# Performance work log

Hardware: AMD Instinct MI355X
Metric: run time of the kernel (lower is better)

Reference implementation:

```python
import jax, jax.numpy as jnp
import numpy as np

L1 = 1e-3  # init kwarg l1
EPS_NORM = 1e-12  # torch F.normalize eps


def _l2_normalize(x):
    # F.normalize(x, p=2, dim=1)
    n = jnp.linalg.norm(x, axis=1, keepdims=True)
    return x / jnp.maximum(n, EPS_NORM)


def _rbf_kernel(x):
    # x: [n, d]
    x2 = jnp.sum(x * x, axis=1, keepdims=True)          # [n,1]
    dist = x2 + x2.T - 2.0 * (x @ x.T)                   # [n,n]
    dist = jnp.maximum(dist, 0.0)
    # torch.median on even-size input returns the LOWER middle element
    flat = jnp.sort(jax.lax.stop_gradient(dist).ravel())
    median_dist = flat[(flat.shape[0] - 1) // 2]
    sigma2 = median_dist + 1e-5
    return jnp.exp(-dist / (2.0 * sigma2))


def _hsic(x, y):
    # x, y: [n, d]. Note: original normalizes in forward AND in hsic; L2
    # normalization is idempotent, so one normalize here is exact.
    x = _l2_normalize(x)
    y = _l2_normalize(y)
    K = _rbf_kernel(x)
    L = _rbf_kernel(y)
    n = K.shape[0]
    # K @ H with H = I - 1/n  ==  K - row_mean(K)
    KH = K - jnp.mean(K, axis=1, keepdims=True)
    LH = L - jnp.mean(L, axis=1, keepdims=True)
    return jnp.sum(KH * LH.T) / float((n - 1) ** 2)


def setup_inputs() -> dict:
    key = jax.random.key(0)
    k1, k2, k3, k4 = jax.random.split(key, 4)
    N, D = 65536, 512     # patches, feature dim
    K_INST, NS = 256, 32  # instances, samples per instance (== max_bg_samples)
    dp = jax.random.normal(k1, (N, D), dtype=jnp.float32)
    gate = jax.random.normal(k2, (N, D), dtype=jnp.float32)
    inst_idx = jax.random.randint(k3, (K_INST, NS), 0, N, dtype=jnp.int64)
    bg_idx = jax.random.randint(k4, (K_INST, NS), 0, N, dtype=jnp.int64)
    return {"dp": dp, "gate": gate, "inst_idx": inst_idx, "bg_idx": bg_idx}


def reference(dp, gate, inst_idx, bg_idx):
    x = dp[inst_idx]   # [K, n, d] per-instance foreground samples
    bg = dp[bg_idx]    # [K, n, d] per-instance background samples
    hs = jax.vmap(_hsic)(x, bg)  # [K]
    return jnp.mean(hs) + L1 * jnp.mean(jnp.abs(gate))
```

## Files before the change

### kernel.cpp

```cpp
#include <hip/hip_runtime.h>
#include <hip/hip_bf16.h>

#define NS 32
#define FD 512
#define K_INST 256
#define CHUNK 256
#define C4 (CHUNK/4)
#define PADF 260
#define PAD4 (PADF/4)
#define MPAD 33
#define GATE_BLOCKS 1024
#define GATE_N4 (65536*512/4)

__device__ __forceinline__ float wave_reduce_add(float v) {
  for (int off = 32; off; off >>= 1) v += __shfl_down(v, off, 64);
  return v;
}

__global__ __launch_bounds__(256) void fused_kernel(
    const float* __restrict__ dp, const float* __restrict__ gate,
    const int* __restrict__ inst_idx, const int* __restrict__ bg_idx,
    float* __restrict__ ws_gate, float* __restrict__ ws_hs) {

  __shared__ float sX[NS * PADF];
  __shared__ float sDist[NS * MPAD];
  __shared__ float sMat[2][NS * MPAD];
  __shared__ float sRowM[2][NS];
  __shared__ float sInv[NS];
  __shared__ float sN2[NS];
  __shared__ int   sIdx[NS];
  __shared__ int   sHist[256];
  __shared__ int   sWaveSum[4];
  __shared__ float sWaveRed[4];
  __shared__ unsigned sPrefix;
  __shared__ int   sWant;

  const int tid  = threadIdx.x;
  const int bid  = blockIdx.x;
  const int lane = tid & 63;
  const int wave = tid >> 6;

  if (bid >= K_INST) {
    const int gb = bid - K_INST;
    const float4* g4 = reinterpret_cast<const float4*>(gate);
    float s = 0.f;
    for (size_t i = (size_t)gb * 256 + tid; i < (size_t)GATE_N4; i += (size_t)GATE_BLOCKS * 256) {
      float4 v = g4[i];
      s += fabsf(v.x) + fabsf(v.y) + fabsf(v.z) + fabsf(v.w);
    }
    s = wave_reduce_add(s);
    if (lane == 0) sWaveRed[wave] = s;
    __syncthreads();
    if (tid == 0) ws_gate[gb] = sWaveRed[0] + sWaveRed[1] + sWaveRed[2] + sWaveRed[3];
    return;
  }

  const int k  = bid;
  const int ti = tid >> 4;
  const int tj = tid & 15;
  const float4* sX4 = reinterpret_cast<const float4*>(sX);

  for (int m = 0; m < 2; ++m) {
    const int* idx = (m == 0 ? inst_idx : bg_idx) + k * NS;
    if (tid < NS) sIdx[tid] = idx[tid];
    __syncthreads();

    float a00 = 0.f, a01 = 0.f, a10 = 0.f, a11 = 0.f;
    for (int ch = 0; ch < 2; ++ch) {
      for (int q = tid; q < NS * C4; q += 256) {
        int r = q >> 6, c = q & 63;
        float4 v = *(reinterpret_cast<const float4*>(dp + (size_t)sIdx[r] * FD + ch * CHUNK) + c);
        *(reinterpret_cast<float4*>(&sX[r * PADF]) + c) = v;
      }
      __syncthreads();
      #pragma unroll 4
      for (int c = 0; c < C4; ++c) {
        float4 x0 = sX4[ti * PAD4 + c];
        float4 x1 = sX4[(ti + 16) * PAD4 + c];
        float4 y0 = sX4[tj * PAD4 + c];
        float4 y1 = sX4[(tj + 16) * PAD4 + c];
        a00 += x0.x*y0.x + x0.y*y0.y + x0.z*y0.z + x0.w*y0.w;
        a01 += x0.x*y1.x + x0.y*y1.y + x0.z*y1.z + x0.w*y1.w;
        a10 += x1.x*y0.x + x1.y*y0.y + x1.z*y0.z + x1.w*y0.w;
        a11 += x1.x*y1.x + x1.y*y1.y + x1.z*y1.z + x1.w*y1.w;
      }
      __syncthreads();
    }

    if (ti == tj) { sN2[ti] = a00; sN2[ti + 16] = a11; }
    __syncthreads();
    if (tid < NS) sInv[tid] = 1.f / fmaxf(sqrtf(sN2[tid]), 1e-12f);
    __syncthreads();

    {
      float i0 = sInv[ti], i1 = sInv[ti + 16], j0 = sInv[tj], j1 = sInv[tj + 16];
      sDist[ti * MPAD + tj]             = (ti == tj) ? 0.f : fmaxf(2.f - 2.f * a00 * i0 * j0, 0.f);
      sDist[ti * MPAD + (tj + 16)]      = fmaxf(2.f - 2.f * a01 * i0 * j1, 0.f);
      sDist[(ti + 16) * MPAD + tj]      = fmaxf(2.f - 2.f * a10 * i1 * j0, 0.f);
      sDist[(ti + 16) * MPAD + (tj + 16)] = (ti == tj) ? 0.f : fmaxf(2.f - 2.f * a11 * i1 * j1, 0.f);
    }
    if (tid == 0) { sPrefix = 0u; sWant = (NS * NS - 1) / 2; }
    __syncthreads();

    for (int shift = 24; shift >= 0; shift -= 8) {
      sHist[tid] = 0;
      __syncthreads();
      unsigned pref = sPrefix;
      int want = sWant;
      unsigned hi_mask = (shift == 24) ? 0u : (0xFFFFFFFFu << (shift + 8));
      for (int q = tid; q < NS * NS; q += 256) {
        unsigned u = __float_as_uint(sDist[(q >> 5) * MPAD + (q & 31)]);
        if ((u & hi_mask) == pref) atomicAdd(&sHist[(u >> shift) & 255], 1);
      }
      __syncthreads();
      int v = sHist[tid];
      int x = v;
      for (int off = 1; off < 64; off <<= 1) {
        int y = __shfl_up(x, off, 64);
        if (lane >= off) x += y;
      }
      if (lane == 63) sWaveSum[wave] = x;
      __syncthreads();
      int add = 0;
      for (int w = 0; w < wave; ++w) add += sWaveSum[w];
      x += add;
      int ex = x - v;
      if (ex <= want && want < ex + v) {
        sPrefix = pref | ((unsigned)tid << shift);
        sWant   = want - ex;
      }
      __syncthreads();
    }
    float sigma2 = __uint_as_float(sPrefix) + 1e-5f;

    for (int q = tid; q < NS * NS; q += 256) {
      int i = q >> 5, j = q & 31;
      sMat[m][i * MPAD + j] = expf(-sDist[i * MPAD + j] / (2.f * sigma2));
    }
    __syncthreads();

    {
      int r = tid >> 3, g = tid & 7;
      float p = 0.f;
      for (int s = 0; s < 4; ++s) p += sMat[m][r * MPAD + g + 8 * s];
      for (int off = 4; off; off >>= 1) p += __shfl_down(p, off, 8);
      if (g == 0) sRowM[m][r] = p * (1.f / 32.f);
    }
    __syncthreads();
  }

  float part = 0.f;
  for (int q = tid; q < NS * NS; q += 256) {
    int i = q >> 5, j = q & 31;
    part += (sMat[0][i * MPAD + j] - sRowM[0][i]) * (sMat[1][i * MPAD + j] - sRowM[1][j]);
  }
  part = wave_reduce_add(part);
  if (lane == 0) sWaveRed[wave] = part;
  __syncthreads();
  if (tid == 0)
    ws_hs[k] = (sWaveRed[0] + sWaveRed[1] + sWaveRed[2] + sWaveRed[3]) * (1.f / 961.f);
}

__global__ __launch_bounds__(256) void final_kernel(
    const float* __restrict__ ws_gate, const float* __restrict__ ws_hs,
    float* __restrict__ out) {
  __shared__ float sW[8];
  const int tid = threadIdx.x, lane = tid & 63, wave = tid >> 6;
  float g = 0.f;
  for (int i = tid; i < GATE_BLOCKS; i += 256) g += ws_gate[i];
  g = wave_reduce_add(g);
  if (lane == 0) sW[wave] = g;
  float h = (tid < K_INST) ? ws_hs[tid] : 0.f;
  h = wave_reduce_add(h);
  if (lane == 0) sW[4 + wave] = h;
  __syncthreads();
  if (tid == 0) {
    float gsum = sW[0] + sW[1] + sW[2] + sW[3];
    float hsum = sW[4] + sW[5] + sW[6] + sW[7];
    out[0] = hsum * (1.f / 256.f) + 1e-3f * (gsum / (65536.f * 512.f));
  }
}

extern "C" void kernel_launch(void* const* d_in, const int* in_sizes, int n_in,
                              void* d_out, int out_size, void* d_ws, size_t ws_size,
                              hipStream_t stream) {
  const float* dp   = (const float*)d_in[0];
  const float* gate = (const float*)d_in[1];
  const int*   inst = (const int*)d_in[2];
  const int*   bg   = (const int*)d_in[3];
  float* out = (float*)d_out;
  float* ws  = (float*)d_ws;
  float* ws_gate = ws;
  float* ws_hs   = ws + GATE_BLOCKS;

  fused_kernel<<<K_INST + GATE_BLOCKS, 256, 0, stream>>>(dp, gate, inst, bg, ws_gate, ws_hs);
  final_kernel<<<1, 256, 0, stream>>>(ws_gate, ws_hs, out);
}
```

Before: 43.43 us.

## Fuse final reduction via last-block counter and restructure Gram tile computation

Replaces the separate final reduction kernel with a last-block-done atomic counter inside the fused kernel; a memset of the counter is added instead. The Gram matrix computation is restructured: each wave handles a quarter of the feature columns with a 4x4 register tile per lane, using an XOR-swizzled unpadded shared layout, register prefetch of the second feature chunk during the first chunk's compute, and a cross-wave partial-sum reduction. The gate loop gets a fixed trip count with unrolling. This trades an extra memset launch and more registers for one fewer kernel launch and better load/compute overlap.

```diff
diff --git a/kernel.cpp b/kernel.cpp
--- a/kernel.cpp
+++ b/kernel.cpp
@@ -5,11 +5,8 @@
 #define FD 512
 #define K_INST 256
 #define CHUNK 256
-#define C4 (CHUNK/4)
-#define PADF 260
-#define PAD4 (PADF/4)
-#define MPAD 33
 #define GATE_BLOCKS 1024
+#define TOTAL_BLOCKS (K_INST + GATE_BLOCKS)
 #define GATE_N4 (65536*512/4)
 
 __device__ __forceinline__ float wave_reduce_add(float v) {
@@ -20,164 +17,215 @@
 __global__ __launch_bounds__(256) void fused_kernel(
     const float* __restrict__ dp, const float* __restrict__ gate,
     const int* __restrict__ inst_idx, const int* __restrict__ bg_idx,
-    float* __restrict__ ws_gate, float* __restrict__ ws_hs) {
-
-  __shared__ float sX[NS * PADF];
-  __shared__ float sDist[NS * MPAD];
-  __shared__ float sMat[2][NS * MPAD];
-  __shared__ float sRowM[2][NS];
-  __shared__ float sInv[NS];
-  __shared__ float sN2[NS];
-  __shared__ int   sIdx[NS];
-  __shared__ int   sHist[256];
-  __shared__ int   sWaveSum[4];
-  __shared__ float sWaveRed[4];
+    int* __restrict__ ctr,
+    float* __restrict__ ws_gate, float* __restrict__ ws_hs,
+    float* __restrict__ out) {
+
+  __shared__ float4 sX4[NS * 64];
+  __shared__ float  sGD[NS * NS];
+  __shared__ float  sMat[2][NS * NS];
+  __shared__ float  sRowM[2][NS];
+  __shared__ float  sInv[NS];
+  __shared__ int    sIdx[NS];
+  __shared__ int    sHist[256];
+  __shared__ int    sWaveSum[4];
+  __shared__ float  sWaveRed[8];
   __shared__ unsigned sPrefix;
-  __shared__ int   sWant;
+  __shared__ int    sWant;
+  __shared__ int    sLast;
+
+  float* sPartF = reinterpret_cast<float*>(sX4);
 
   const int tid  = threadIdx.x;
   const int bid  = blockIdx.x;
   const int lane = tid & 63;
-  const int wave = tid >> 6;
+  const int w    = tid >> 6;
 
   if (bid >= K_INST) {
     const int gb = bid - K_INST;
     const float4* g4 = reinterpret_cast<const float4*>(gate);
     float s = 0.f;
-    for (size_t i = (size_t)gb * 256 + tid; i < (size_t)GATE_N4; i += (size_t)GATE_BLOCKS * 256) {
-      float4 v = g4[i];
+    size_t base = (size_t)gb * 256 + tid;
+    #pragma unroll 4
+    for (int it = 0; it < 32; ++it) {
+      float4 v = g4[base + (size_t)it * (GATE_BLOCKS * 256)];
       s += fabsf(v.x) + fabsf(v.y) + fabsf(v.z) + fabsf(v.w);
     }
     s = wave_reduce_add(s);
-    if (lane == 0) sWaveRed[wave] = s;
+    if (lane == 0) sWaveRed[w] = s;
     __syncthreads();
     if (tid == 0) ws_gate[gb] = sWaveRed[0] + sWaveRed[1] + sWaveRed[2] + sWaveRed[3];
-    return;
-  }
-
-  const int k  = bid;
-  const int ti = tid >> 4;
-  const int tj = tid & 15;
-  const float4* sX4 = reinterpret_cast<const float4*>(sX);
-
-  for (int m = 0; m < 2; ++m) {
-    const int* idx = (m == 0 ? inst_idx : bg_idx) + k * NS;
-    if (tid < NS) sIdx[tid] = idx[tid];
-    __syncthreads();
-
-    float a00 = 0.f, a01 = 0.f, a10 = 0.f, a11 = 0.f;
-    for (int ch = 0; ch < 2; ++ch) {
-      for (int q = tid; q < NS * C4; q += 256) {
-        int r = q >> 6, c = q & 63;
-        float4 v = *(reinterpret_cast<const float4*>(dp + (size_t)sIdx[r] * FD + ch * CHUNK) + c);
-        *(reinterpret_cast<float4*>(&sX[r * PADF]) + c) = v;
-      }
-      __syncthreads();
+  } else {
+    const int k  = bid;
+    const int li = lane >> 3;
+    const int lj = lane & 7;
+
+    for (int m = 0; m < 2; ++m) {
+      const int* idx = (m == 0 ? inst_idx : bg_idx) + k * NS;
+      if (tid < NS) sIdx[tid] = idx[tid];
+      __syncthreads();
+
+      float acc[4][4];
+      #pragma unroll
+      for (int a = 0; a < 4; ++a)
+        #pragma unroll
+        for (int b = 0; b < 4; ++b) acc[a][b] = 0.f;
+
+      float4 pre[8];
+      #pragma unroll
+      for (int kk = 0; kk < 8; ++kk) {
+        int r = w + 4 * kk;
+        pre[kk] = *(reinterpret_cast<const float4*>(dp + (size_t)sIdx[r] * FD) + lane);
+      }
+      #pragma unroll
+      for (int kk = 0; kk < 8; ++kk) {
+        int r = w + 4 * kk;
+        sX4[r * 64 + (lane ^ (r & 7))] = pre[kk];
+      }
+      __syncthreads();
+      #pragma unroll
+      for (int kk = 0; kk < 8; ++kk) {
+        int r = w + 4 * kk;
+        pre[kk] = *(reinterpret_cast<const float4*>(dp + (size_t)sIdx[r] * FD + CHUNK) + lane);
+      }
       #pragma unroll 4
-      for (int c = 0; c < C4; ++c) {
-        float4 x0 = sX4[ti * PAD4 + c];
-        float4 x1 = sX4[(ti + 16) * PAD4 + c];
-        float4 y0 = sX4[tj * PAD4 + c];
-        float4 y1 = sX4[(tj + 16) * PAD4 + c];
-        a00 += x0.x*y0.x + x0.y*y0.y + x0.z*y0.z + x0.w*y0.w;
-        a01 += x0.x*y1.x + x0.y*y1.y + x0.z*y1.z + x0.w*y1.w;
-        a10 += x1.x*y0.x + x1.y*y0.y + x1.z*y0.z + x1.w*y0.w;
-        a11 += x1.x*y1.x + x1.y*y1.y + x1.z*y1.z + x1.w*y1.w;
-      }
-      __syncthreads();
-    }
-
-    if (ti == tj) { sN2[ti] = a00; sN2[ti + 16] = a11; }
-    __syncthreads();
-    if (tid < NS) sInv[tid] = 1.f / fmaxf(sqrtf(sN2[tid]), 1e-12f);
-    __syncthreads();
-
-    {
-      float i0 = sInv[ti], i1 = sInv[ti + 16], j0 = sInv[tj], j1 = sInv[tj + 16];
-      sDist[ti * MPAD + tj]             = (ti == tj) ? 0.f : fmaxf(2.f - 2.f * a00 * i0 * j0, 0.f);
-      sDist[ti * MPAD + (tj + 16)]      = fmaxf(2.f - 2.f * a01 * i0 * j1, 0.f);
-      sDist[(ti + 16) * MPAD + tj]      = fmaxf(2.f - 2.f * a10 * i1 * j0, 0.f);
-      sDist[(ti + 16) * MPAD + (tj + 16)] = (ti == tj) ? 0.f : fmaxf(2.f - 2.f * a11 * i1 * j1, 0.f);
-    }
-    if (tid == 0) { sPrefix = 0u; sWant = (NS * NS - 1) / 2; }
-    __syncthreads();
-
-    for (int shift = 24; shift >= 0; shift -= 8) {
-      sHist[tid] = 0;
-      __syncthreads();
-      unsigned pref = sPrefix;
-      int want = sWant;
-      unsigned hi_mask = (shift == 24) ? 0u : (0xFFFFFFFFu << (shift + 8));
-      for (int q = tid; q < NS * NS; q += 256) {
-        unsigned u = __float_as_uint(sDist[(q >> 5) * MPAD + (q & 31)]);
-        if ((u & hi_mask) == pref) atomicAdd(&sHist[(u >> shift) & 255], 1);
-      }
-      __syncthreads();
-      int v = sHist[tid];
-      int x = v;
-      for (int off = 1; off < 64; off <<= 1) {
-        int y = __shfl_up(x, off, 64);
-        if (lane >= off) x += y;
-      }
-      if (lane == 63) sWaveSum[wave] = x;
-      __syncthreads();
-      int add = 0;
-      for (int w = 0; w < wave; ++w) add += sWaveSum[w];
-      x += add;
-      int ex = x - v;
-      if (ex <= want && want < ex + v) {
-        sPrefix = pref | ((unsigned)tid << shift);
-        sWant   = want - ex;
-      }
-      __syncthreads();
-    }
-    float sigma2 = __uint_as_float(sPrefix) + 1e-5f;
-
+      for (int c = 16 * w; c < 16 * w + 16; ++c) {
+        float4 xs[4], ys[4];
+        #pragma unroll
+        for (int s = 0; s < 4; ++s) {
+          xs[s] = sX4[(li + 8 * s) * 64 + (c ^ li)];
+          ys[s] = sX4[(lj + 8 * s) * 64 + (c ^ lj)];
+        }
+        #pragma unroll
+        for (int a = 0; a < 4; ++a)
+          #pragma unroll
+          for (int b = 0; b < 4; ++b)
+            acc[a][b] += xs[a].x * ys[b].x + xs[a].y * ys[b].y
+                       + xs[a].z * ys[b].z + xs[a].w * ys[b].w;
+      }
+      __syncthreads();
+      #pragma unroll
+      for (int kk = 0; kk < 8; ++kk) {
+        int r = w + 4 * kk;
+        sX4[r * 64 + (lane ^ (r & 7))] = pre[kk];
+      }
+      __syncthreads();
+      #pragma unroll 4
+      for (int c = 16 * w; c < 16 * w + 16; ++c) {
+        float4 xs[4], ys[4];
+        #pragma unroll
+        for (int s = 0; s < 4; ++s) {
+          xs[s] = sX4[(li + 8 * s) * 64 + (c ^ li)];
+          ys[s] = sX4[(lj + 8 * s) * 64 + (c ^ lj)];
+        }
+        #pragma unroll
+        for (int a = 0; a < 4; ++a)
+          #pragma unroll
+          for (int b = 0; b < 4; ++b)
+            acc[a][b] += xs[a].x * ys[b].x + xs[a].y * ys[b].y
+                       + xs[a].z * ys[b].z + xs[a].w * ys[b].w;
+      }
+      __syncthreads();
+      #pragma unroll
+      for (int a = 0; a < 4; ++a)
+        #pragma unroll
+        for (int b = 0; b < 4; ++b) {
+          int A = li + 8 * a, B = lj + 8 * b;
+          sPartF[w * 1024 + A * 32 + (B ^ ((A & 3) << 3))] = acc[a][b];
+        }
+      __syncthreads();
+      for (int p = tid; p < 1024; p += 256) {
+        float s = sPartF[p] + sPartF[1024 + p] + sPartF[2048 + p] + sPartF[3072 + p];
+        int A = p >> 5, Bx = p & 31;
+        sGD[A * 32 + (Bx ^ ((A & 3) << 3))] = s;
+      }
+      __syncthreads();
+      if (tid < NS) sInv[tid] = 1.f / fmaxf(sqrtf(sGD[tid * 33]), 1e-12f);
+      __syncthreads();
+      for (int p = tid; p < 1024; p += 256) {
+        int i = p >> 5, j = p & 31;
+        sGD[p] = (i == j) ? 0.f
+                          : fmaxf(2.f - 2.f * sGD[p] * sInv[i] * sInv[j], 0.f);
+      }
+      if (tid == 0) { sPrefix = 0u; sWant = (NS * NS - 1) / 2; }
+      __syncthreads();
+
+      for (int shift = 24; shift >= 0; shift -= 8) {
+        sHist[tid] = 0;
+        __syncthreads();
+        unsigned pref = sPrefix;
+        int want = sWant;
+        unsigned hi_mask = (shift == 24) ? 0u : (0xFFFFFFFFu << (shift + 8));
+        for (int q = tid; q < NS * NS; q += 256) {
+          unsigned u = __float_as_uint(sGD[q]);
+          if ((u & hi_mask) == pref) atomicAdd(&sHist[(u >> shift) & 255], 1);
+        }
+        __syncthreads();
+        int v = sHist[tid];
+        int x = v;
+        for (int off = 1; off < 64; off <<= 1) {
+          int y = __shfl_up(x, off, 64);
+          if (lane >= off) x += y;
+        }
+        if (lane == 63) sWaveSum[w] = x;
+        __syncthreads();
+        int add = 0;
+        for (int ww = 0; ww < w; ++ww) add += sWaveSum[ww];
+        x += add;
+        int ex = x - v;
+        if (ex <= want && want < ex + v) {
+          sPrefix = pref | ((unsigned)tid << shift);
+          sWant   = want - ex;
+        }
+        __syncthreads();
+      }
+      float sigma2 = __uint_as_float(sPrefix) + 1e-5f;
+
+      for (int q = tid; q < NS * NS; q += 256)
+        sMat[m][q] = expf(-sGD[q] / (2.f * sigma2));
+      __syncthreads();
+      {
+        int r = tid >> 3, g = tid & 7;
+        float p = 0.f;
+        for (int s = 0; s < 4; ++s) p += sMat[m][r * 32 + g + 8 * s];
+        for (int off = 4; off; off >>= 1) p += __shfl_down(p, off, 8);
+        if (g == 0) sRowM[m][r] = p * (1.f / 32.f);
+      }
+      __syncthreads();
+    }
+
+    float part = 0.f;
     for (int q = tid; q < NS * NS; q += 256) {
       int i = q >> 5, j = q & 31;
-      sMat[m][i * MPAD + j] = expf(-sDist[i * MPAD + j] / (2.f * sigma2));
-    }
+      part += (sMat[0][q] - sRowM[0][i]) * (sMat[1][q] - sRowM[1][j]);
+    }
+    part = wave_reduce_add(part);
+    if (lane == 0) sWaveRed[w] = part;
     __syncthreads();
-
-    {
-      int r = tid >> 3, g = tid & 7;
-      float p = 0.f;
-      for (int s = 0; s < 4; ++s) p += sMat[m][r * MPAD + g + 8 * s];
-      for (int off = 4; off; off >>= 1) p += __shfl_down(p, off, 8);
-      if (g == 0) sRowM[m][r] = p * (1.f / 32.f);
-    }
+    if (tid == 0)
+      ws_hs[k] = (sWaveRed[0] + sWaveRed[1] + sWaveRed[2] + sWaveRed[3]) * (1.f / 961.f);
+  }
+
+  if (tid == 0) {
+    __threadfence();
+    sLast = (atomicAdd(ctr, 1) == TOTAL_BLOCKS - 1) ? 1 : 0;
+  }
+  __syncthreads();
+  if (sLast) {
+    __threadfence();
+    float g = 0.f;
+    for (int i = tid; i < GATE_BLOCKS; i += 256) g += ws_gate[i];
+    g = wave_reduce_add(g);
+    if (lane == 0) sWaveRed[w] = g;
+    float h = (tid < K_INST) ? ws_hs[tid] : 0.f;
+    h = wave_reduce_add(h);
+    if (lane == 0) sWaveRed[4 + w] = h;
     __syncthreads();
-  }
-
-  float part = 0.f;
-  for (int q = tid; q < NS * NS; q += 256) {
-    int i = q >> 5, j = q & 31;
-    part += (sMat[0][i * MPAD + j] - sRowM[0][i]) * (sMat[1][i * MPAD + j] - sRowM[1][j]);
-  }
-  part = wave_reduce_add(part);
-  if (lane == 0) sWaveRed[wave] = part;
-  __syncthreads();
-  if (tid == 0)
-    ws_hs[k] = (sWaveRed[0] + sWaveRed[1] + sWaveRed[2] + sWaveRed[3]) * (1.f / 961.f);
-}
-
-__global__ __launch_bounds__(256) void final_kernel(
-    const float* __restrict__ ws_gate, const float* __restrict__ ws_hs,
-    float* __restrict__ out) {
-  __shared__ float sW[8];
-  const int tid = threadIdx.x, lane = tid & 63, wave = tid >> 6;
-  float g = 0.f;
-  for (int i = tid; i < GATE_BLOCKS; i += 256) g += ws_gate[i];
-  g = wave_reduce_add(g);
-  if (lane == 0) sW[wave] = g;
-  float h = (tid < K_INST) ? ws_hs[tid] : 0.f;
-  h = wave_reduce_add(h);
-  if (lane == 0) sW[4 + wave] = h;
-  __syncthreads();
-  if (tid == 0) {
-    float gsum = sW[0] + sW[1] + sW[2] + sW[3];
-    float hsum = sW[4] + sW[5] + sW[6] + sW[7];
-    out[0] = hsum * (1.f / 256.f) + 1e-3f * (gsum / (65536.f * 512.f));
+    if (tid == 0) {
+      float gsum = sWaveRed[0] + sWaveRed[1] + sWaveRed[2] + sWaveRed[3];
+      float hsum = sWaveRed[4] + sWaveRed[5] + sWaveRed[6] + sWaveRed[7];
+      out[0] = hsum * (1.f / 256.f) + 1e-3f * (gsum / (65536.f * 512.f));
+    }
   }
 }
 
@@ -190,9 +238,10 @@
   const int*   bg   = (const int*)d_in[3];
   float* out = (float*)d_out;
   float* ws  = (float*)d_ws;
-  float* ws_gate = ws;
-  float* ws_hs   = ws + GATE_BLOCKS;
-
-  fused_kernel<<<K_INST + GATE_BLOCKS, 256, 0, stream>>>(dp, gate, inst, bg, ws_gate, ws_hs);
-  final_kernel<<<1, 256, 0, stream>>>(ws_gate, ws_hs, out);
+  int*   ctr = (int*)d_ws;
+  float* ws_gate = ws + 16;
+  float* ws_hs   = ws + 16 + GATE_BLOCKS;
+
+  hipMemsetAsync(d_ws, 0, 4, stream);
+  fused_kernel<<<TOTAL_BLOCKS, 256, 0, stream>>>(dp, gate, inst, bg, ctr, ws_gate, ws_hs, out);
 }
```

Result: slower. 84.12 us (+93.7%).

## Split HSIC per-matrix work across two blocks and add contraction kernel

Applied to the files above, without the earlier changes.

Each instance's K and L kernel-matrix computations now run in separate blocks (512 HSIC blocks instead of 256), which halves the serial per-block chain of gather, Gram, radix median select and exp. The resulting 32x32 matrices and row means are written to workspace, and a new contract_kernel computes the centered HSIC sum per instance. This exposes more parallelism on the long-latency HSIC path. The cost is an extra kernel launch plus a round trip of about 2 MB through global memory.

```diff
diff --git a/kernel.cpp b/kernel.cpp
--- a/kernel.cpp
+++ b/kernel.cpp
@@ -9,6 +9,7 @@
 #define PADF 260
 #define PAD4 (PADF/4)
 #define MPAD 33
+#define HSIC_BLOCKS 512
 #define GATE_BLOCKS 1024
 #define GATE_N4 (65536*512/4)
 
@@ -20,12 +21,12 @@
 __global__ __launch_bounds__(256) void fused_kernel(
     const float* __restrict__ dp, const float* __restrict__ gate,
     const int* __restrict__ inst_idx, const int* __restrict__ bg_idx,
-    float* __restrict__ ws_gate, float* __restrict__ ws_hs) {
+    float* __restrict__ ws_gate, float* __restrict__ ws_mats,
+    float* __restrict__ ws_means) {
 
   __shared__ float sX[NS * PADF];
-  __shared__ float sDist[NS * MPAD];
-  __shared__ float sMat[2][NS * MPAD];
-  __shared__ float sRowM[2][NS];
+  __shared__ float sD[NS * MPAD];
+  __shared__ float sRowM[NS];
   __shared__ float sInv[NS];
   __shared__ float sN2[NS];
   __shared__ int   sIdx[NS];
@@ -38,10 +39,10 @@
   const int tid  = threadIdx.x;
   const int bid  = blockIdx.x;
   const int lane = tid & 63;
-  const int wave = tid >> 6;
-
-  if (bid >= K_INST) {
-    const int gb = bid - K_INST;
+  const int w    = tid >> 6;
+
+  if (bid >= HSIC_BLOCKS) {
+    const int gb = bid - HSIC_BLOCKS;
     const float4* g4 = reinterpret_cast<const float4*>(gate);
     float s = 0.f;
     for (size_t i = (size_t)gb * 256 + tid; i < (size_t)GATE_N4; i += (size_t)GATE_BLOCKS * 256) {
@@ -49,113 +50,129 @@
       s += fabsf(v.x) + fabsf(v.y) + fabsf(v.z) + fabsf(v.w);
     }
     s = wave_reduce_add(s);
-    if (lane == 0) sWaveRed[wave] = s;
+    if (lane == 0) sWaveRed[w] = s;
     __syncthreads();
     if (tid == 0) ws_gate[gb] = sWaveRed[0] + sWaveRed[1] + sWaveRed[2] + sWaveRed[3];
     return;
   }
 
-  const int k  = bid;
+  const int k = bid >> 1;
+  const int m = bid & 1;
   const int ti = tid >> 4;
   const int tj = tid & 15;
   const float4* sX4 = reinterpret_cast<const float4*>(sX);
 
-  for (int m = 0; m < 2; ++m) {
-    const int* idx = (m == 0 ? inst_idx : bg_idx) + k * NS;
-    if (tid < NS) sIdx[tid] = idx[tid];
-    __syncthreads();
-
-    float a00 = 0.f, a01 = 0.f, a10 = 0.f, a11 = 0.f;
-    for (int ch = 0; ch < 2; ++ch) {
-      for (int q = tid; q < NS * C4; q += 256) {
-        int r = q >> 6, c = q & 63;
-        float4 v = *(reinterpret_cast<const float4*>(dp + (size_t)sIdx[r] * FD + ch * CHUNK) + c);
-        *(reinterpret_cast<float4*>(&sX[r * PADF]) + c) = v;
-      }
-      __syncthreads();
-      #pragma unroll 4
-      for (int c = 0; c < C4; ++c) {
-        float4 x0 = sX4[ti * PAD4 + c];
-        float4 x1 = sX4[(ti + 16) * PAD4 + c];
-        float4 y0 = sX4[tj * PAD4 + c];
-        float4 y1 = sX4[(tj + 16) * PAD4 + c];
-        a00 += x0.x*y0.x + x0.y*y0.y + x0.z*y0.z + x0.w*y0.w;
-        a01 += x0.x*y1.x + x0.y*y1.y + x0.z*y1.z + x0.w*y1.w;
-        a10 += x1.x*y0.x + x1.y*y0.y + x1.z*y0.z + x1.w*y0.w;
-        a11 += x1.x*y1.x + x1.y*y1.y + x1.z*y1.z + x1.w*y1.w;
-      }
-      __syncthreads();
-    }
-
-    if (ti == tj) { sN2[ti] = a00; sN2[ti + 16] = a11; }
-    __syncthreads();
-    if (tid < NS) sInv[tid] = 1.f / fmaxf(sqrtf(sN2[tid]), 1e-12f);
-    __syncthreads();
-
-    {
-      float i0 = sInv[ti], i1 = sInv[ti + 16], j0 = sInv[tj], j1 = sInv[tj + 16];
-      sDist[ti * MPAD + tj]             = (ti == tj) ? 0.f : fmaxf(2.f - 2.f * a00 * i0 * j0, 0.f);
-      sDist[ti * MPAD + (tj + 16)]      = fmaxf(2.f - 2.f * a01 * i0 * j1, 0.f);
-      sDist[(ti + 16) * MPAD + tj]      = fmaxf(2.f - 2.f * a10 * i1 * j0, 0.f);
-      sDist[(ti + 16) * MPAD + (tj + 16)] = (ti == tj) ? 0.f : fmaxf(2.f - 2.f * a11 * i1 * j1, 0.f);
-    }
-    if (tid == 0) { sPrefix = 0u; sWant = (NS * NS - 1) / 2; }
-    __syncthreads();
-
-    for (int shift = 24; shift >= 0; shift -= 8) {
-      sHist[tid] = 0;
-      __syncthreads();
-      unsigned pref = sPrefix;
-      int want = sWant;
-      unsigned hi_mask = (shift == 24) ? 0u : (0xFFFFFFFFu << (shift + 8));
-      for (int q = tid; q < NS * NS; q += 256) {
-        unsigned u = __float_as_uint(sDist[(q >> 5) * MPAD + (q & 31)]);
-        if ((u & hi_mask) == pref) atomicAdd(&sHist[(u >> shift) & 255], 1);
-      }
-      __syncthreads();
-      int v = sHist[tid];
-      int x = v;
-      for (int off = 1; off < 64; off <<= 1) {
-        int y = __shfl_up(x, off, 64);
-        if (lane >= off) x += y;
-      }
-      if (lane == 63) sWaveSum[wave] = x;
-      __syncthreads();
-      int add = 0;
-      for (int w = 0; w < wave; ++w) add += sWaveSum[w];
-      x += add;
-      int ex = x - v;
-      if (ex <= want && want < ex + v) {
-        sPrefix = pref | ((unsigned)tid << shift);
-        sWant   = want - ex;
-      }
-      __syncthreads();
-    }
-    float sigma2 = __uint_as_float(sPrefix) + 1e-5f;
-
+  const int* idx = (m == 0 ? inst_idx : bg_idx) + k * NS;
+  if (tid < NS) sIdx[tid] = idx[tid];
+  __syncthreads();
+
+  float a00 = 0.f, a01 = 0.f, a10 = 0.f, a11 = 0.f;
+  for (int ch = 0; ch < 2; ++ch) {
+    for (int q = tid; q < NS * C4; q += 256) {
+      int r = q >> 6, c = q & 63;
+      float4 v = *(reinterpret_cast<const float4*>(dp + (size_t)sIdx[r] * FD + ch * CHUNK) + c);
+      *(reinterpret_cast<float4*>(&sX[r * PADF]) + c) = v;
+    }
+    __syncthreads();
+    #pragma unroll 4
+    for (int c = 0; c < C4; ++c) {
+      float4 x0 = sX4[ti * PAD4 + c];
+      float4 x1 = sX4[(ti + 16) * PAD4 + c];
+      float4 y0 = sX4[tj * PAD4 + c];
+      float4 y1 = sX4[(tj + 16) * PAD4 + c];
+      a00 += x0.x*y0.x + x0.y*y0.y + x0.z*y0.z + x0.w*y0.w;
+      a01 += x0.x*y1.x + x0.y*y1.y + x0.z*y1.z + x0.w*y1.w;
+      a10 += x1.x*y0.x + x1.y*y0.y + x1.z*y0.z + x1.w*y0.w;
+      a11 += x1.x*y1.x + x1.y*y1.y + x1.z*y1.z + x1.w*y1.w;
+    }
+    __syncthreads();
+  }
+
+  if (ti == tj) { sN2[ti] = a00; sN2[ti + 16] = a11; }
+  __syncthreads();
+  if (tid < NS) sInv[tid] = 1.f / fmaxf(sqrtf(sN2[tid]), 1e-12f);
+  __syncthreads();
+
+  {
+    float i0 = sInv[ti], i1 = sInv[ti + 16], j0 = sInv[tj], j1 = sInv[tj + 16];
+    sD[ti * MPAD + tj]               = (ti == tj) ? 0.f : fmaxf(2.f - 2.f * a00 * i0 * j0, 0.f);
+    sD[ti * MPAD + (tj + 16)]        = fmaxf(2.f - 2.f * a01 * i0 * j1, 0.f);
+    sD[(ti + 16) * MPAD + tj]        = fmaxf(2.f - 2.f * a10 * i1 * j0, 0.f);
+    sD[(ti + 16) * MPAD + (tj + 16)] = (ti == tj) ? 0.f : fmaxf(2.f - 2.f * a11 * i1 * j1, 0.f);
+  }
+  if (tid == 0) { sPrefix = 0u; sWant = (NS * NS - 1) / 2; }
+  __syncthreads();
+
+  for (int shift = 24; shift >= 0; shift -= 8) {
+    sHist[tid] = 0;
+    __syncthreads();
+    unsigned pref = sPrefix;
+    int want = sWant;
+    unsigned hi_mask = (shift == 24) ? 0u : (0xFFFFFFFFu << (shift + 8));
     for (int q = tid; q < NS * NS; q += 256) {
-      int i = q >> 5, j = q & 31;
-      sMat[m][i * MPAD + j] = expf(-sDist[i * MPAD + j] / (2.f * sigma2));
-    }
-    __syncthreads();
-
-    {
-      int r = tid >> 3, g = tid & 7;
-      float p = 0.f;
-      for (int s = 0; s < 4; ++s) p += sMat[m][r * MPAD + g + 8 * s];
-      for (int off = 4; off; off >>= 1) p += __shfl_down(p, off, 8);
-      if (g == 0) sRowM[m][r] = p * (1.f / 32.f);
-    }
-    __syncthreads();
-  }
-
+      unsigned u = __float_as_uint(sD[(q >> 5) * MPAD + (q & 31)]);
+      if ((u & hi_mask) == pref) atomicAdd(&sHist[(u >> shift) & 255], 1);
+    }
+    __syncthreads();
+    int v = sHist[tid];
+    int x = v;
+    for (int off = 1; off < 64; off <<= 1) {
+      int y = __shfl_up(x, off, 64);
+      if (lane >= off) x += y;
+    }
+    if (lane == 63) sWaveSum[w] = x;
+    __syncthreads();
+    int add = 0;
+    for (int ww = 0; ww < w; ++ww) add += sWaveSum[ww];
+    x += add;
+    int ex = x - v;
+    if (ex <= want && want < ex + v) {
+      sPrefix = pref | ((unsigned)tid << shift);
+      sWant   = want - ex;
+    }
+    __syncthreads();
+  }
+  float sigma2 = __uint_as_float(sPrefix) + 1e-5f;
+
+  for (int q = tid; q < NS * NS; q += 256) {
+    int i = q >> 5, j = q & 31;
+    sD[i * MPAD + j] = expf(-sD[i * MPAD + j] / (2.f * sigma2));
+  }
+  __syncthreads();
+
+  {
+    int r = tid >> 3, g = tid & 7;
+    float p = 0.f;
+    for (int s = 0; s < 4; ++s) p += sD[r * MPAD + g + 8 * s];
+    for (int off = 4; off; off >>= 1) p += __shfl_down(p, off, 8);
+    if (g == 0) sRowM[r] = p * (1.f / 32.f);
+  }
+  __syncthreads();
+
+  float* mat = ws_mats + (size_t)bid * 1024;
+  for (int q = tid; q < NS * NS; q += 256)
+    mat[q] = sD[(q >> 5) * MPAD + (q & 31)];
+  if (tid < NS) ws_means[bid * NS + tid] = sRowM[tid];
+}
+
+__global__ __launch_bounds__(256) void contract_kernel(
+    const float* __restrict__ ws_mats, const float* __restrict__ ws_means,
+    float* __restrict__ ws_hs) {
+  __shared__ float sRM[2][NS];
+  __shared__ float sWaveRed[4];
+  const int k = blockIdx.x;
+  const int tid = threadIdx.x, lane = tid & 63, w = tid >> 6;
+  const float* Km = ws_mats + (size_t)(k * 2 + 0) * 1024;
+  const float* Lm = ws_mats + (size_t)(k * 2 + 1) * 1024;
+  if (tid < 64) sRM[tid >> 5][tid & 31] = ws_means[(k * 2 + (tid >> 5)) * NS + (tid & 31)];
+  __syncthreads();
   float part = 0.f;
   for (int q = tid; q < NS * NS; q += 256) {
     int i = q >> 5, j = q & 31;
-    part += (sMat[0][i * MPAD + j] - sRowM[0][i]) * (sMat[1][i * MPAD + j] - sRowM[1][j]);
+    part += (Km[q] - sRM[0][i]) * (Lm[q] - sRM[1][j]);
   }
   part = wave_reduce_add(part);
-  if (lane == 0) sWaveRed[wave] = part;
+  if (lane == 0) sWaveRed[w] = part;
   __syncthreads();
   if (tid == 0)
     ws_hs[k] = (sWaveRed[0] + sWaveRed[1] + sWaveRed[2] + sWaveRed[3]) * (1.f / 961.f);
@@ -190,9 +207,13 @@
   const int*   bg   = (const int*)d_in[3];
   float* out = (float*)d_out;
   float* ws  = (float*)d_ws;
-  float* ws_gate = ws;
-  float* ws_hs   = ws + GATE_BLOCKS;
-
-  fused_kernel<<<K_INST + GATE_BLOCKS, 256, 0, stream>>>(dp, gate, inst, bg, ws_gate, ws_hs);
+  float* ws_gate  = ws;
+  float* ws_hs    = ws + 1024;
+  float* ws_means = ws + 1024 + 256;
+  float* ws_mats  = ws + 1024 + 256 + 512 * 32;
+
+  fused_kernel<<<HSIC_BLOCKS + GATE_BLOCKS, 256, 0, stream>>>(
+      dp, gate, inst, bg, ws_gate, ws_mats, ws_means);
+  contract_kernel<<<K_INST, 256, 0, stream>>>(ws_mats, ws_means, ws_hs);
   final_kernel<<<1, 256, 0, stream>>>(ws_gate, ws_hs, out);
 }
```

After: 38.01 us. 12.5% less time.
